# Kernel tuning notes

Hardware: AMD Instinct MI355X
Metric: run time of the kernel (lower is better)

Reference implementation:

```python
import jax, jax.numpy as jnp
import numpy as np

B = 8192   # batch of trajectories
T = 32     # time points
H = 256    # hidden_dim
NL = 4     # num_layers
EPS = 1e-5 # LayerNorm eps (torch default)


def setup_inputs() -> dict:
    key = jax.random.key(0)
    ks = jax.random.split(key, 8)
    # xavier-ish scales (gain 0.5 for hidden, 0.1 for output, per _init_weights)
    s0 = 0.5 * np.sqrt(2.0 / (6 + H))
    sh = 0.5 * np.sqrt(2.0 / (H + H))
    so = 0.1 * np.sqrt(2.0 / (H + 3))
    return {
        "y0": jax.random.normal(ks[0], (B, 3), dtype=jnp.float32),
        "t_span": jnp.arange(T, dtype=jnp.float32) * 0.01,
        "params": jax.random.uniform(ks[1], (B, 3), dtype=jnp.float32),  # [Omega, Delta, gamma] > 0
        "W0": jax.random.normal(ks[2], (6, H), dtype=jnp.float32) * s0,
        "b0": jnp.zeros((H,), dtype=jnp.float32),
        "Wh": jax.random.normal(ks[3], (NL - 1, H, H), dtype=jnp.float32) * sh,
        "bh": jnp.zeros((NL - 1, H), dtype=jnp.float32),
        "ln_g": jnp.ones((NL, H), dtype=jnp.float32),
        "ln_b": jnp.zeros((NL, H), dtype=jnp.float32),
        "Wout": jax.random.normal(ks[4], (H, 3), dtype=jnp.float32) * so,
        "bout": jnp.zeros((3,), dtype=jnp.float32),
        "gate": jnp.float32(0.5),
    }


def _layernorm(h, g, b):
    mu = jnp.mean(h, axis=-1, keepdims=True)
    var = jnp.mean(jnp.square(h - mu), axis=-1, keepdims=True)
    return (h - mu) * jax.lax.rsqrt(var + EPS) * g + b


def reference(y0, t_span, params, W0, b0, Wh, bh, ln_g, ln_b, Wout, bout, gate):
    def correction_net(y, p):
        # input: concat([u,v,w, Omega,Delta,gamma]) -> (B, 6)
        h = jnp.concatenate([y, p], axis=-1) @ W0 + b0
        h = jax.nn.silu(_layernorm(h, ln_g[0], ln_b[0]))
        for i in range(NL - 1):
            h = jax.nn.silu(_layernorm(h @ Wh[i] + bh[i], ln_g[i + 1], ln_b[i + 1]))
        return h @ Wout + bout  # (B, 3)

    def bloch_rhs_incomplete(y, p):
        u, v, w = y[:, 0:1], y[:, 1:2], y[:, 2:3]
        Om, ga = p[:, 0:1], p[:, 2:3]
        du = -ga * u
        dv = -ga * v - Om * w
        dw = -2.0 * ga * (w + 1.0) + Om * v
        return jnp.concatenate([du, dv, dw], axis=-1)

    def f_total(y):
        return bloch_rhs_incomplete(y, params) + gate * correction_net(y, params)

    def rk4_step(y, dt):
        k1 = f_total(y)
        k2 = f_total(y + 0.5 * dt * k1)
        k3 = f_total(y + 0.5 * dt * k2)
        k4 = f_total(y + dt * k3)
        y_new = y + (dt / 6.0) * (k1 + 2.0 * k2 + 2.0 * k3 + k4)
        return y_new, y_new

    dts = jnp.diff(t_span)              # (T-1,)
    _, ys = jax.lax.scan(rk4_step, y0, dts)
    return jnp.concatenate([y0[None], ys], axis=0)  # (T, B, 3)
```

## Files before the change

### kernel.cpp

```cpp
#include <hip/hip_runtime.h>

typedef unsigned short u16;
typedef short v8s   __attribute__((ext_vector_type(8)));
typedef float f32x4 __attribute__((ext_vector_type(4)));
typedef float f32x2 __attribute__((ext_vector_type(2)));

#define H_ 256
#define B_ 8192
#define NSTEP 31
#define NTHREADS 512
#define NBLOCKS 256
#define AROW 264

#define MFMA16(a,b,c) __builtin_amdgcn_mfma_f32_16x16x32_bf16(a,b,c,0,0,0)

#define DPP_QP_XOR1 0xB1
#define DPP_QP_XOR2 0x4E
#define DPP_ROR4    0x124
#define DPP_ROR8    0x128

template<int CTRL>
__device__ __forceinline__ float dpp_add(float v){
  return v + __int_as_float(
      __builtin_amdgcn_update_dpp(0, __float_as_int(v), CTRL, 0xF, 0xF, true));
}

__device__ __forceinline__ float bperm(float v, int srclane){
  return __int_as_float(
      __builtin_amdgcn_ds_bpermute(srclane*4, __float_as_int(v)));
}

__device__ __forceinline__ u16 f2bf_rne(float f){
  unsigned u = __float_as_uint(f);
  u += 0x7fffu + ((u >> 16) & 1u);
  return (u16)(u >> 16);
}
__device__ __forceinline__ u16 f2bf_trunc(float f){
  return (u16)(__float_as_uint(f) >> 16);
}

#define WS_W0   0
#define WS_W1   8192
#define WS_W23  73728
#define WS_WO   204800
#define WS_TOT  205824

__global__ void prep_kernel(const float* __restrict__ W0,
                            const float* __restrict__ b0,
                            const float* __restrict__ Wh,
                            const float* __restrict__ Wout,
                            u16* __restrict__ ws){
  int i = blockIdx.x * 256 + threadIdx.x;
  if (i < 8192){
    int q = i >> 11, n = (i >> 3) & 255, j = i & 7;
    int k = q*8 + j;
    float v = (k < 6) ? W0[k*H_ + n] : ((k == 6) ? b0[n] : 0.f);
    ws[i] = f2bf_rne(v);
  } else if (i < 73728){
    int r = i - 8192;
    int n = r >> 8, k = r & 255;
    ws[i] = f2bf_rne(Wh[k*H_ + n]);
  } else if (i < 204800){
    int r = i - 73728;
    int l = r >> 16, r2 = r & 65535;
    int kc = r2 >> 13, r3 = r2 & 8191;
    int q = r3 >> 11, n = (r3 >> 3) & 255, j = r3 & 7;
    int k = kc*32 + q*8 + j;
    ws[i] = f2bf_rne(Wh[(1 + l)*H_*H_ + k*H_ + n]);
  } else if (i < WS_TOT){
    int r = i - 204800;
    int kc = r >> 7, q = (r >> 5) & 3, nn = (r >> 3) & 3, j = r & 7;
    int k = kc*32 + q*8 + j;
    ws[i] = f2bf_rne(nn < 3 ? Wout[k*3 + nn] : 0.f);
  }
}

#define PWROW 10
#define OFF_A      0
#define OFF_W1     16896
#define OFF_WOUT   152064
#define OFF_PART   154112
#define OFF_MR     156672
#define OFF_NET    156928
#define OFF_YCUR   157440
#define OFF_YSUM   157952
#define OFF_YSTG   158464
#define OFF_P      158976
#define OFF_DTS    159488
#define LDS_TOTAL  159616

__global__ __launch_bounds__(NTHREADS, 2)
void pinode_kernel(const float* __restrict__ y0g, const float* __restrict__ t_span,
                   const float* __restrict__ params, const float* __restrict__ bhg,
                   const float* __restrict__ ln_gg, const float* __restrict__ ln_bg,
                   const float* __restrict__ boutg, const float* __restrict__ gatep,
                   const u16* __restrict__ ws, float* __restrict__ out)
{
  extern __shared__ char smem[];
  u16*   A    = (u16*)(smem + OFF_A);
  u16*   W1   = (u16*)(smem + OFF_W1);
  u16*   WO   = (u16*)(smem + OFF_WOUT);
  float* part = (float*)(smem + OFF_PART);
  float* net  = (float*)(smem + OFF_NET);
  float* ycur = (float*)(smem + OFF_YCUR);
  float* ysum = (float*)(smem + OFF_YSUM);
  float* ystg = (float*)(smem + OFF_YSTG);
  float* pL   = (float*)(smem + OFF_P);
  float* dts  = (float*)(smem + OFF_DTS);

  const int tid = threadIdx.x;
  const int wave = tid >> 6;
  const int lane = tid & 63;
  const int q    = lane >> 4;
  const int c15  = lane & 15;
  const int colbase = wave * 32;
  const int s0 = blockIdx.x * 32;

  for (int idx = tid; idx < 8192; idx += NTHREADS){
    int n = idx >> 5, ch = idx & 31;
    *(v8s*)(W1 + n*AROW + ch*8) = *(const v8s*)(ws + WS_W1 + n*256 + ch*8);
  }
  if (tid < 128)
    *(v8s*)(WO + tid*8) = *(const v8s*)(ws + WS_WO + tid*8);
  if (tid < 96){
    int s = tid & 31, c = tid >> 5;
    float y = y0g[(s0+s)*3 + c];
    ycur[s*4+c] = y; ystg[s*4+c] = y;
    pL[s*4+c]   = params[(s0+s)*3 + c];
    out[(s0+s)*3 + c] = y;
  }
  if (tid < NSTEP) dts[tid] = t_span[tid+1] - t_span[tid];

  v8s wf[2][8][2];
#pragma unroll
  for (int l = 0; l < 2; ++l)
#pragma unroll
    for (int kc = 0; kc < 8; ++kc)
#pragma unroll
      for (int nt = 0; nt < 2; ++nt)
        wf[l][kc][nt] = *(const v8s*)(ws + WS_W23 +
            (((l*8 + kc)*4 + q)*256 + colbase + nt*16 + c15)*8);

  v8s w0f[2];
#pragma unroll
  for (int nt = 0; nt < 2; ++nt)
    w0f[nt] = *(const v8s*)(ws + WS_W0 + (q*256 + colbase + nt*16 + c15)*8);

  float lng[4][2], lnb[4][2], bia[4][2];
#pragma unroll
  for (int l = 0; l < 4; ++l)
#pragma unroll
    for (int nt = 0; nt < 2; ++nt){
      int col = colbase + nt*16 + c15;
      lng[l][nt] = ln_gg[l*H_ + col];
      lnb[l][nt] = ln_bg[l*H_ + col];
      bia[l][nt] = (l == 0) ? 0.f : bhg[(l-1)*H_ + col];
    }
  const float gate = gatep[0];
  const float bo0 = boutg[0], bo1 = boutg[1], bo2 = boutg[2];
  const f32x4 fzero = {0.f, 0.f, 0.f, 0.f};

  const u16* pa  = A + c15*AROW + q*8;
  const u16* pw  = W1 + (colbase + c15)*AROW + q*8;
  u16* pstA = A + (q*4)*AROW + colbase + c15;

  __syncthreads();

  {
    int s = tid >> 4, pr = tid & 15;
    int e0 = pr*2, e1 = e0 + 1;
    float x0 = (e0 < 3) ? ystg[s*4+e0] : ((e0 < 6) ? pL[s*4+e0-3] : (e0 == 6 ? 1.f : 0.f));
    float x1 = (e1 < 3) ? ystg[s*4+e1] : ((e1 < 6) ? pL[s*4+e1-3] : (e1 == 6 ? 1.f : 0.f));
    unsigned pk = (unsigned)f2bf_rne(x0) | ((unsigned)f2bf_rne(x1) << 16);
    *(unsigned*)(A + s*AROW + e0) = pk;
  }
  __syncthreads();

  auto ln_silu = [&](f32x4 (&acc)[2][2], int li){
    float rs[2][4], rq[2][4];
#pragma unroll
    for (int mt = 0; mt < 2; ++mt)
#pragma unroll
      for (int r = 0; r < 4; ++r){
        float a0 = acc[mt][0][r], a1 = acc[mt][1][r];
        rs[mt][r] = a0 + a1;
        rq[mt][r] = a0*a0 + a1*a1;
      }
#pragma unroll
    for (int mt = 0; mt < 2; ++mt)
#pragma unroll
      for (int r = 0; r < 4; ++r){
        float s = rs[mt][r], qq = rq[mt][r];
        s = dpp_add<DPP_QP_XOR1>(s);  qq = dpp_add<DPP_QP_XOR1>(qq);
        s = dpp_add<DPP_QP_XOR2>(s);  qq = dpp_add<DPP_QP_XOR2>(qq);
        s = dpp_add<DPP_ROR4>(s);     qq = dpp_add<DPP_ROR4>(qq);
        s = dpp_add<DPP_ROR8>(s);     qq = dpp_add<DPP_ROR8>(qq);
        rs[mt][r] = s; rq[mt][r] = qq;
      }
    if (c15 == 0){
#pragma unroll
      for (int mt = 0; mt < 2; ++mt)
#pragma unroll
        for (int r = 0; r < 4; ++r){
          int row = mt*16 + q*4 + r;
          f32x2 v; v.x = rs[mt][r]; v.y = rq[mt][r];
          *(f32x2*)(part + (row*PWROW + wave)*2) = v;
        }
    }
    __syncthreads();
    float rstd_my, mb_my;
    {
      const f32x4* pp = (const f32x4*)(part + (lane & 31)*PWROW*2);
      f32x4 p0 = pp[0], p1 = pp[1], p2 = pp[2], p3 = pp[3];
      float S = p0[0]+p0[2]+p1[0]+p1[2]+p2[0]+p2[2]+p3[0]+p3[2];
      float Q = p0[1]+p0[3]+p1[1]+p1[3]+p2[1]+p2[3]+p3[1]+p3[3];
      float mean = S * (1.f/256.f);
      float var  = Q * (1.f/256.f) - mean*mean;
      rstd_my = rsqrtf(var + 1e-5f);
      mb_my   = -mean * rstd_my;
    }
#pragma unroll
    for (int mt = 0; mt < 2; ++mt)
#pragma unroll
      for (int r = 0; r < 4; ++r){
        int row = mt*16 + q*4 + r;
        float rstd = bperm(rstd_my, row);
        float mb   = bperm(mb_my, row);
#pragma unroll
        for (int nt = 0; nt < 2; ++nt){
          float t  = acc[mt][nt][r] * rstd + mb;
          float v  = t * lng[li][nt] + lnb[li][nt];
          float e  = __builtin_amdgcn_exp2f(v * -1.44269504f);
          float sv = v * __builtin_amdgcn_rcpf(1.f + e);
          pstA[(mt*16 + r)*AROW + nt*16] = f2bf_trunc(sv);
        }
      }
    __syncthreads();
  };

#pragma unroll 1
  for (int step = 0; step < NSTEP; ++step){
    float dt = dts[step];
#pragma unroll 1
    for (int stage = 0; stage < 4; ++stage){
      f32x4 acc[2][2];

#pragma unroll
      for (int mt = 0; mt < 2; ++mt)
#pragma unroll
        for (int nt = 0; nt < 2; ++nt) acc[mt][nt] = fzero;
      {
        v8s a0 = *(const v8s*)(pa);
        v8s a1 = *(const v8s*)(pa + 16*AROW);
        acc[0][0] = MFMA16(a0, w0f[0], acc[0][0]);
        acc[0][1] = MFMA16(a0, w0f[1], acc[0][1]);
        acc[1][0] = MFMA16(a1, w0f[0], acc[1][0]);
        acc[1][1] = MFMA16(a1, w0f[1], acc[1][1]);
      }
      ln_silu(acc, 0);

#pragma unroll
      for (int mt = 0; mt < 2; ++mt)
#pragma unroll
        for (int nt = 0; nt < 2; ++nt) acc[mt][nt] = fzero;
#pragma unroll
      for (int kc = 0; kc < 8; ++kc){
        v8s a0 = *(const v8s*)(pa + kc*32);
        v8s a1 = *(const v8s*)(pa + 16*AROW + kc*32);
        v8s bb0 = *(const v8s*)(pw + kc*32);
        v8s bb1 = *(const v8s*)(pw + 16*AROW + kc*32);
        acc[0][0] = MFMA16(a0, bb0, acc[0][0]);
        acc[0][1] = MFMA16(a0, bb1, acc[0][1]);
        acc[1][0] = MFMA16(a1, bb0, acc[1][0]);
        acc[1][1] = MFMA16(a1, bb1, acc[1][1]);
      }
#pragma unroll
      for (int mt = 0; mt < 2; ++mt)
#pragma unroll
        for (int nt = 0; nt < 2; ++nt)
#pragma unroll
          for (int r = 0; r < 4; ++r) acc[mt][nt][r] += bia[1][nt];
      ln_silu(acc, 1);

#pragma unroll
      for (int l = 0; l < 2; ++l){
#pragma unroll
        for (int mt = 0; mt < 2; ++mt)
#pragma unroll
          for (int nt = 0; nt < 2; ++nt) acc[mt][nt] = fzero;
#pragma unroll
        for (int kc = 0; kc < 8; ++kc){
          v8s a0 = *(const v8s*)(pa + kc*32);
          v8s a1 = *(const v8s*)(pa + 16*AROW + kc*32);
          acc[0][0] = MFMA16(a0, wf[l][kc][0], acc[0][0]);
          acc[0][1] = MFMA16(a0, wf[l][kc][1], acc[0][1]);
          acc[1][0] = MFMA16(a1, wf[l][kc][0], acc[1][0]);
          acc[1][1] = MFMA16(a1, wf[l][kc][1], acc[1][1]);
        }
#pragma unroll
        for (int mt = 0; mt < 2; ++mt)
#pragma unroll
          for (int nt = 0; nt < 2; ++nt)
#pragma unroll
            for (int r = 0; r < 4; ++r) acc[mt][nt][r] += bia[2+l][nt];
        ln_silu(acc, 2+l);
      }

      if (wave < 2){
        f32x4 ao = fzero;
        int nn = c15 < 3 ? c15 : 3;
#pragma unroll
        for (int kc = 0; kc < 8; ++kc){
          v8s a = *(const v8s*)(A + (wave*16 + c15)*AROW + kc*32 + q*8);
          v8s b = *(const v8s*)(WO + ((kc*4 + q)*4 + nn)*8);
          ao = MFMA16(a, b, ao);
        }
        if (c15 < 3){
#pragma unroll
          for (int r = 0; r < 4; ++r)
            net[(wave*16 + q*4 + r)*4 + c15] = ao[r];
        }
      }
      __syncthreads();

      if (tid < 32){
        int s = tid;
        float u = ystg[s*4+0], v = ystg[s*4+1], w = ystg[s*4+2];
        float Om = pL[s*4+0], ga = pL[s*4+2];
        float kk[3];
        kk[0] = -ga*u                      + gate*(net[s*4+0] + bo0);
        kk[1] = -ga*v - Om*w               + gate*(net[s*4+1] + bo1);
        kk[2] = -2.f*ga*(w + 1.f) + Om*v   + gate*(net[s*4+2] + bo2);
#pragma unroll
        for (int c = 0; c < 3; ++c){
          float yc = ycur[s*4+c];
          float k  = kk[c];
          float ys;
          if (stage == 3){
            float accw = ysum[s*4+c] + dt*(1.f/6.f)*k;
            ycur[s*4+c] = accw;
            ys = accw;
            out[(step+1)*(B_*3) + (s0+s)*3 + c] = accw;
          } else {
            float accw = (stage == 0) ? (yc + dt*(1.f/6.f)*k)
                                      : (ysum[s*4+c] + dt*(1.f/3.f)*k);
            ysum[s*4+c] = accw;
            ys = yc + ((stage == 2) ? dt : 0.5f*dt)*k;
          }
          ystg[s*4+c] = ys;
          A[s*AROW + c] = f2bf_rne(ys);
          A[s*AROW + 3 + c] = f2bf_rne(pL[s*4+c]);
        }
        *(unsigned*)(A + s*AROW + 6) = 0x00003F80u;
      }
      __syncthreads();
    }
  }
}

extern "C" void kernel_launch(void* const* d_in, const int* in_sizes, int n_in,
                              void* d_out, int out_size, void* d_ws, size_t ws_size,
                              hipStream_t stream) {
  const float* y0     = (const float*)d_in[0];
  const float* t_span = (const float*)d_in[1];
  const float* params = (const float*)d_in[2];
  const float* W0     = (const float*)d_in[3];
  const float* b0     = (const float*)d_in[4];
  const float* Wh     = (const float*)d_in[5];
  const float* bh     = (const float*)d_in[6];
  const float* ln_g   = (const float*)d_in[7];
  const float* ln_b   = (const float*)d_in[8];
  const float* Wout   = (const float*)d_in[9];
  const float* bout   = (const float*)d_in[10];
  const float* gate   = (const float*)d_in[11];
  float* out = (float*)d_out;
  u16* ws = (u16*)d_ws;

  prep_kernel<<<WS_TOT/256, 256, 0, stream>>>(W0, b0, Wh, Wout, ws);

  hipFuncSetAttribute(reinterpret_cast<const void*>(pinode_kernel),
                      hipFuncAttributeMaxDynamicSharedMemorySize, LDS_TOTAL);
  pinode_kernel<<<NBLOCKS, NTHREADS, LDS_TOTAL, stream>>>(
      y0, t_span, params, bh, ln_g, ln_b, bout, gate, ws, out);
}
```

Baseline: 1.113 ms.

## Compute output projection and RK update redundantly in every wave, dropping a barrier

Every wave now computes the full 32-row output projection with MFMA and performs the RK4 stage update in its own lanes. Before, only two waves computed the projection and one 32-thread group did the update between two barriers. The RK state buffers (ycur, ysum, ystg) are double-buffered by stage parity, which removes the net staging buffer and one __syncthreads per stage. The price is redundant MFMA and LDS work in all waves, plus identical concurrent writes to A and the state buffers, which depend on later barriers for correctness.

```diff
diff --git a/kernel.cpp b/kernel.cpp
--- a/kernel.cpp
+++ b/kernel.cpp
@@ -80,14 +80,12 @@
 #define OFF_W1     16896
 #define OFF_WOUT   152064
 #define OFF_PART   154112
-#define OFF_MR     156672
-#define OFF_NET    156928
-#define OFF_YCUR   157440
-#define OFF_YSUM   157952
-#define OFF_YSTG   158464
-#define OFF_P      158976
-#define OFF_DTS    159488
-#define LDS_TOTAL  159616
+#define OFF_YCUR   156672
+#define OFF_YSUM   157696
+#define OFF_YSTG   158720
+#define OFF_P      159744
+#define OFF_DTS    160256
+#define LDS_TOTAL  160384
 
 __global__ __launch_bounds__(NTHREADS, 2)
 void pinode_kernel(const float* __restrict__ y0g, const float* __restrict__ t_span,
@@ -101,7 +99,6 @@
   u16*   W1   = (u16*)(smem + OFF_W1);
   u16*   WO   = (u16*)(smem + OFF_WOUT);
   float* part = (float*)(smem + OFF_PART);
-  float* net  = (float*)(smem + OFF_NET);
   float* ycur = (float*)(smem + OFF_YCUR);
   float* ysum = (float*)(smem + OFF_YSUM);
   float* ystg = (float*)(smem + OFF_YSTG);
@@ -113,6 +110,7 @@
   const int lane = tid & 63;
   const int q    = lane >> 4;
   const int c15  = lane & 15;
+  const int nn   = (c15 < 3) ? c15 : 3;
   const int colbase = wave * 32;
   const int s0 = blockIdx.x * 32;
 
@@ -306,54 +304,63 @@
         ln_silu(acc, 2+l);
       }
 
-      if (wave < 2){
-        f32x4 ao = fzero;
-        int nn = c15 < 3 ? c15 : 3;
+      {
+        const int cur = (stage & 1)*128, nx = ((stage & 1) ^ 1)*128;
+        f32x4 ao0 = fzero, ao1 = fzero;
 #pragma unroll
         for (int kc = 0; kc < 8; ++kc){
-          v8s a = *(const v8s*)(A + (wave*16 + c15)*AROW + kc*32 + q*8);
-          v8s b = *(const v8s*)(WO + ((kc*4 + q)*4 + nn)*8);
-          ao = MFMA16(a, b, ao);
+          v8s b  = *(const v8s*)(WO + ((kc*4 + q)*4 + nn)*8);
+          v8s a0 = *(const v8s*)(pa + kc*32);
+          v8s a1 = *(const v8s*)(pa + 16*AROW + kc*32);
+          ao0 = MFMA16(a0, b, ao0);
+          ao1 = MFMA16(a1, b, ao1);
+        }
+        if (c15 == 3){
+#pragma unroll
+          for (int m = 0; m < 2; ++m)
+#pragma unroll
+            for (int r = 0; r < 4; ++r){
+              int s = m*16 + q*4 + r;
+              *(unsigned*)(A + s*AROW + 6) = 0x00003F80u;
+            }
         }
         if (c15 < 3){
-#pragma unroll
-          for (int r = 0; r < 4; ++r)
-            net[(wave*16 + q*4 + r)*4 + c15] = ao[r];
-        }
-      }
-      __syncthreads();
-
-      if (tid < 32){
-        int s = tid;
-        float u = ystg[s*4+0], v = ystg[s*4+1], w = ystg[s*4+2];
-        float Om = pL[s*4+0], ga = pL[s*4+2];
-        float kk[3];
-        kk[0] = -ga*u                      + gate*(net[s*4+0] + bo0);
-        kk[1] = -ga*v - Om*w               + gate*(net[s*4+1] + bo1);
-        kk[2] = -2.f*ga*(w + 1.f) + Om*v   + gate*(net[s*4+2] + bo2);
-#pragma unroll
-        for (int c = 0; c < 3; ++c){
-          float yc = ycur[s*4+c];
-          float k  = kk[c];
-          float ys;
-          if (stage == 3){
-            float accw = ysum[s*4+c] + dt*(1.f/6.f)*k;
-            ycur[s*4+c] = accw;
-            ys = accw;
-            out[(step+1)*(B_*3) + (s0+s)*3 + c] = accw;
-          } else {
-            float accw = (stage == 0) ? (yc + dt*(1.f/6.f)*k)
-                                      : (ysum[s*4+c] + dt*(1.f/3.f)*k);
-            ysum[s*4+c] = accw;
-            ys = yc + ((stage == 2) ? dt : 0.5f*dt)*k;
+          const int c = c15;
+          const float boc = (c == 0) ? bo0 : ((c == 1) ? bo1 : bo2);
+#pragma unroll
+          for (int m = 0; m < 2; ++m){
+            f32x4 ao = m ? ao1 : ao0;
+#pragma unroll
+            for (int r = 0; r < 4; ++r){
+              int s = m*16 + q*4 + r;
+              float Om = pL[s*4+0], ga = pL[s*4+2];
+              float yi  = ystg[cur + s*4+c];
+              float oth = ystg[cur + s*4 + ((c == 1) ? 2 : 1)];
+              float kA = (c == 2) ? (Om*oth - 2.f*ga*(yi + 1.f))
+                                  : (-ga*yi - ((c == 1) ? Om*oth : 0.f));
+              float kk = kA + gate*(ao[r] + boc);
+              float yc = ycur[cur + s*4+c];
+              float ys, ycn;
+              if (stage == 3){
+                float acw = ysum[cur + s*4+c] + dt*(1.f/6.f)*kk;
+                ycn = acw; ys = acw;
+                ysum[nx + s*4+c] = acw;
+                if (wave == 0) out[(step+1)*(B_*3) + (s0+s)*3 + c] = acw;
+              } else {
+                float acw = (stage == 0) ? (yc + dt*(1.f/6.f)*kk)
+                                         : (ysum[cur + s*4+c] + dt*(1.f/3.f)*kk);
+                ysum[nx + s*4+c] = acw;
+                ycn = yc;
+                ys = yc + ((stage == 2) ? dt : 0.5f*dt)*kk;
+              }
+              ycur[nx + s*4+c] = ycn;
+              ystg[nx + s*4+c] = ys;
+              A[s*AROW + c] = f2bf_rne(ys);
+              A[s*AROW + 3 + c] = f2bf_rne(pL[s*4+c]);
+            }
           }
-          ystg[s*4+c] = ys;
-          A[s*AROW + c] = f2bf_rne(ys);
-          A[s*AROW + 3 + c] = f2bf_rne(pL[s*4+c]);
-        }
-        *(unsigned*)(A + s*AROW + 6) = 0x00003F80u;
-      }
-      __syncthreads();
+        }
+      }
     }
   }
 }
```

After: 2.118 ms. 90.4% more time.
